# Optimization experiments

Hardware: AMD Instinct MI355X
Metric: run time of the kernel (lower is better)

Reference implementation:

```python
import jax, jax.numpy as jnp
import numpy as np

D_MODEL = 1024
N_HEADS = 16
HEAD_DIM = D_MODEL // N_HEADS


def setup_inputs() -> dict:
    key = jax.random.key(0)
    ks = jax.random.split(key, 9)
    B, S, D = 2, 2048, D_MODEL
    scale = 1.0 / np.sqrt(D)
    return {
        "q": jax.random.normal(ks[0], (B, S, D), jnp.float32),
        "k": jax.random.normal(ks[1], (B, S, D), jnp.float32),
        "v": jax.random.normal(ks[2], (B, S, D), jnp.float32),
        "Wq": jax.random.normal(ks[3], (D, D), jnp.float32) * scale,
        "bq": jax.random.normal(ks[4], (D,), jnp.float32) * 0.01,
        "Wk": jax.random.normal(ks[5], (D, D), jnp.float32) * scale,
        "bk": jax.random.normal(ks[6], (D,), jnp.float32) * 0.01,
        "Wv": jax.random.normal(ks[7], (D, D), jnp.float32) * scale,
        "bv": jax.random.normal(ks[8], (D,), jnp.float32) * 0.01,
    }


def reference(q, k, v, Wq, bq, Wk, bk, Wv, bv):
    B, S, D = q.shape
    H, Dh = N_HEADS, D // N_HEADS
    # linear projections (torch Linear: x @ W.T + b)
    qp = q @ Wq.T + bq
    kp = k @ Wk.T + bk
    vp = v @ Wv.T + bv
    # [B, S, H, Dh] -> [B, H, S, Dh]
    qh = qp.reshape(B, S, H, Dh).transpose(0, 2, 1, 3)
    kh = kp.reshape(B, S, H, Dh).transpose(0, 2, 1, 3)
    vh = vp.reshape(B, S, H, Dh).transpose(0, 2, 1, 3)
    # scaled dot-product attention (mask=None path)
    scores = jnp.einsum('bhqd,bhkd->bhqk', qh, kh) / jnp.sqrt(jnp.asarray(Dh, qh.dtype))
    attn = jax.nn.softmax(scores, axis=-1)
    out = jnp.einsum('bhqk,bhkd->bhqd', attn, vh)
    # [B, H, S, Dh] -> [B, S, D]
    return out.transpose(0, 2, 1, 3).reshape(B, S, D)
```

## Files before the change

### kernel.cpp

```cpp
#include <hip/hip_runtime.h>
#include <stdint.h>
#include <stddef.h>


#define NH  16
#define DH  64
#define SEQ 2048
#define DM  1024
#define NB  2

#define ACT_N (NB * SEQ * DM)
#define W_N   (DM * DM)
#define QSCALE 0.18033688011116012f

typedef float  f32x4  __attribute__((ext_vector_type(4)));
typedef __bf16 bf16x8 __attribute__((ext_vector_type(8)));
typedef __bf16 bf16x4 __attribute__((ext_vector_type(4)));

__device__ __forceinline__ __bf16 f2bf(float f) { return (__bf16)f; }

__device__ __forceinline__ float fexp2(float x) {
    float r; asm("v_exp_f32 %0, %1" : "=v"(r) : "v"(x)); return r;
}

__device__ __forceinline__ void gload_lds16(const void* g, void* l) {
    __builtin_amdgcn_global_load_lds(
        (const __attribute__((address_space(1))) void*)g,
        (__attribute__((address_space(3))) void*)l, 16, 0, 0);
}

__global__ __launch_bounds__(256) void cvt6(
    const float* __restrict__ s0, const float* __restrict__ s1,
    const float* __restrict__ s2, const float* __restrict__ s3,
    const float* __restrict__ s4, const float* __restrict__ s5,
    __bf16* __restrict__ d0, __bf16* __restrict__ d1, __bf16* __restrict__ d2,
    __bf16* __restrict__ d3, __bf16* __restrict__ d4, __bf16* __restrict__ d5)
{
    const float* s; __bf16* d; int n;
    switch (blockIdx.z) {
        case 0: s = s0; d = d0; n = ACT_N; break;
        case 1: s = s1; d = d1; n = ACT_N; break;
        case 2: s = s2; d = d2; n = ACT_N; break;
        case 3: s = s3; d = d3; n = W_N;   break;
        case 4: s = s4; d = d4; n = W_N;   break;
        default: s = s5; d = d5; n = W_N;  break;
    }
    const size_t i = ((size_t)blockIdx.x * 256 + threadIdx.x) * 8;
    if (i >= (size_t)n) return;
    float4 f0 = *(const float4*)(s + i);
    float4 f1 = *(const float4*)(s + i + 4);
    bf16x8 o;
    o[0] = f2bf(f0.x); o[1] = f2bf(f0.y); o[2] = f2bf(f0.z); o[3] = f2bf(f0.w);
    o[4] = f2bf(f1.x); o[5] = f2bf(f1.y); o[6] = f2bf(f1.z); o[7] = f2bf(f1.w);
    *(bf16x8*)(d + i) = o;
}

__global__ __launch_bounds__(256) void proj3(
    const __bf16* __restrict__ X0, const __bf16* __restrict__ X1, const __bf16* __restrict__ X2,
    const __bf16* __restrict__ W0, const __bf16* __restrict__ W1, const __bf16* __restrict__ W2,
    const float* __restrict__ b0, const float* __restrict__ b1, const float* __restrict__ b2,
    __bf16* __restrict__ dq, __bf16* __restrict__ dk, __bf16* __restrict__ dv)
{
    __shared__ __align__(16) __bf16 sA[128][32];
    __shared__ __align__(16) __bf16 sB[128][32];

    const __bf16 *X, *W; const float* bias; __bf16* dst;
    if (blockIdx.z == 0)      { X = X0; W = W0; bias = b0; dst = dq; }
    else if (blockIdx.z == 1) { X = X1; W = W1; bias = b1; dst = dk; }
    else                      { X = X2; W = W2; bias = b2; dst = dv; }
    const bool vpath = (blockIdx.z == 2);

    const int lane = threadIdx.x & 63;
    const int wv   = threadIdx.x >> 6;
    const int mb = blockIdx.x * 128;
    const int nb = blockIdx.y * 128;
    const int lm0 = (wv >> 1) * 64;
    const int ln0 = (wv & 1) * 64;
    const int lr = lane & 15;
    const int lg = lane >> 4;
    const int lk = lg * 8;
    const int srow = lane >> 2;
    const int scol = (lane & 3) * 8;

    f32x4 acc[4][4];
#pragma unroll
    for (int i = 0; i < 4; ++i)
#pragma unroll
        for (int j = 0; j < 4; ++j) acc[i][j] = (f32x4){0.f, 0.f, 0.f, 0.f};

    for (int k0 = 0; k0 < DM; k0 += 32) {
        __syncthreads();
#pragma unroll
        for (int c = wv * 2; c < wv * 2 + 2; ++c) {
            gload_lds16(X + (size_t)(mb + c * 16 + srow) * DM + k0 + scol, &sA[c * 16][0]);
            gload_lds16(W + (size_t)(nb + c * 16 + srow) * DM + k0 + scol, &sB[c * 16][0]);
        }
        __syncthreads();

        bf16x8 a[4], b[4];
#pragma unroll
        for (int t = 0; t < 4; ++t) {
            a[t] = *(const bf16x8*)&sA[lm0 + t * 16 + lr][lk];
            b[t] = *(const bf16x8*)&sB[ln0 + t * 16 + lr][lk];
        }
        if (!vpath) {
#pragma unroll
            for (int nt = 0; nt < 4; ++nt)
#pragma unroll
                for (int mt = 0; mt < 4; ++mt)
                    acc[nt][mt] = __builtin_amdgcn_mfma_f32_16x16x32_bf16(
                        b[nt], a[mt], acc[nt][mt], 0, 0, 0);
        } else {
#pragma unroll
            for (int mt = 0; mt < 4; ++mt)
#pragma unroll
                for (int nt = 0; nt < 4; ++nt)
                    acc[mt][nt] = __builtin_amdgcn_mfma_f32_16x16x32_bf16(
                        a[mt], b[nt], acc[mt][nt], 0, 0, 0);
        }
    }

    if (!vpath) {
        const float scale = (blockIdx.z == 0) ? QSCALE : 1.0f;
#pragma unroll
        for (int nt = 0; nt < 4; ++nt) {
            const int n_base = nb + ln0 + nt * 16 + lg * 4;
            const float4 bb = *(const float4*)&bias[n_base];
            const int h = n_base >> 6, dh = n_base & 63;
#pragma unroll
            for (int mt = 0; mt < 4; ++mt) {
                const int m_g = mb + lm0 + mt * 16 + lr;
                const int bi = m_g >> 11;
                const int s  = m_g & (SEQ - 1);
                bf16x4 w;
                w[0] = f2bf((acc[nt][mt][0] + bb.x) * scale);
                w[1] = f2bf((acc[nt][mt][1] + bb.y) * scale);
                w[2] = f2bf((acc[nt][mt][2] + bb.z) * scale);
                w[3] = f2bf((acc[nt][mt][3] + bb.w) * scale);
                *(bf16x4*)&dst[((size_t)((bi * NH + h) * SEQ + s)) * DH + dh] = w;
            }
        }
    } else {
        const int h = (nb + ln0) >> 6;
#pragma unroll
        for (int nt = 0; nt < 4; ++nt) {
            const int n_g = nb + ln0 + nt * 16 + lr;
            const float bb = bias[n_g];
            const int dh = n_g & 63;
#pragma unroll
            for (int mt = 0; mt < 4; ++mt) {
                const int m_g = mb + lm0 + mt * 16 + lg * 4;
                const int bi = m_g >> 11;
                const int s0 = m_g & (SEQ - 1);
                bf16x4 w;
#pragma unroll
                for (int r = 0; r < 4; ++r) w[r] = f2bf(acc[mt][nt][r] + bb);
                *(bf16x4*)&dst[((size_t)((bi * NH + h) * DH + dh)) * SEQ + s0] = w;
            }
        }
    }
}

__global__ __launch_bounds__(256) void attn_kernel(
    const __bf16* __restrict__ qh, const __bf16* __restrict__ kh,
    const __bf16* __restrict__ vT, float* __restrict__ out)
{
    __shared__ __align__(16) __bf16 kbuf[3][4096];
    __shared__ __align__(16) __bf16 vbuf[3][4096];

    const int tid  = threadIdx.x;
    const int lane = tid & 63;
    const int wv   = tid >> 6;
    const int i    = blockIdx.x;
    const int slot = i >> 3;
    const int bh   = (i & 7) * 4 + (slot >> 4);
    const int qt   = slot & 15;
    const size_t hb = (size_t)bh * SEQ * DH;
    const int q0 = qt * 128 + wv * 32;
    const int lq = lane & 15;
    const int lg = lane >> 4;
    const int swz = (lq & 7) << 4;

    const int p0 = tid, p1 = tid + 256;
    const int c0 = (p0 ^ ((p0 >> 3) & 7)) & 7;
    const int c1 = (p1 ^ ((p1 >> 3) & 7)) & 7;
    const int r0 = p0 >> 3, r1 = p1 >> 3;
    const int gr0 = (r0 & 35) | ((r0 & 12) << 1) | ((r0 & 16) >> 2);
    const int gr1 = (r1 & 35) | ((r1 & 12) << 1) | ((r1 & 16) >> 2);
    const __bf16* ks0 = kh + hb + (size_t)gr0 * DH + c0 * 8;
    const __bf16* ks1 = kh + hb + (size_t)gr1 * DH + c1 * 8;
    const __bf16* vs0 = vT + hb + (size_t)r0 * SEQ + c0 * 8;
    const __bf16* vs1 = vT + hb + (size_t)r1 * SEQ + c1 * 8;
    const int dst0 = wv * 512;
    const int dst1 = 2048 + wv * 512;

#define STAGE(SEL, TI) { \
    gload_lds16(ks0 + (size_t)(TI) * 64 * DH, &kbuf[SEL][dst0]); \
    gload_lds16(ks1 + (size_t)(TI) * 64 * DH, &kbuf[SEL][dst1]); \
    gload_lds16(vs0 + (TI) * 64, &vbuf[SEL][dst0]); \
    gload_lds16(vs1 + (TI) * 64, &vbuf[SEL][dst1]); }

    bf16x8 bQ[2][2];
#pragma unroll
    for (int qtf = 0; qtf < 2; ++qtf)
#pragma unroll
        for (int ks = 0; ks < 2; ++ks)
            bQ[qtf][ks] = *(const bf16x8*)(qh + hb +
                (size_t)(q0 + qtf * 16 + lq) * DH + ks * 32 + lg * 8);

    bf16x8 ONES;
#pragma unroll
    for (int e = 0; e < 8; ++e) ONES[e] = f2bf(1.0f);

    f32x4 O[2][4];
#pragma unroll
    for (int qtf = 0; qtf < 2; ++qtf)
#pragma unroll
        for (int dt = 0; dt < 4; ++dt) O[qtf][dt] = (f32x4){0.f, 0.f, 0.f, 0.f};
    f32x4 Ol[2];
    Ol[0] = (f32x4){0.f, 0.f, 0.f, 0.f};
    Ol[1] = (f32x4){0.f, 0.f, 0.f, 0.f};

    const int rdk0 = lq * 128 + ((0 * 64 + lg * 16) ^ swz);
    const int rdk1 = lq * 128 + ((1 * 64 + lg * 16) ^ swz);

    f32x4 scA[2][4], scB[2][4];
    bf16x8 paf[2][2];

#define QK(SL, SC) { \
    const char* kc = (const char*)&kbuf[SL][0]; \
    _Pragma("unroll") for (int kt = 0; kt < 4; ++kt) { \
        const bf16x8 ak0 = *(const bf16x8*)(kc + kt * 2048 + rdk0); \
        const bf16x8 ak1 = *(const bf16x8*)(kc + kt * 2048 + rdk1); \
        _Pragma("unroll") for (int qtf = 0; qtf < 2; ++qtf) { \
            f32x4 c = (f32x4){0.f, 0.f, 0.f, 0.f}; \
            c = __builtin_amdgcn_mfma_f32_16x16x32_bf16(ak0, bQ[qtf][0], c, 0, 0, 0); \
            c = __builtin_amdgcn_mfma_f32_16x16x32_bf16(ak1, bQ[qtf][1], c, 0, 0, 0); \
            SC[qtf][kt] = c; } } }

#define SMAX(SC) { \
    _Pragma("unroll") for (int qtf = 0; qtf < 2; ++qtf) \
    _Pragma("unroll") for (int ks = 0; ks < 2; ++ks) { \
        bf16x8 w; \
        _Pragma("unroll") for (int r = 0; r < 4; ++r) { \
            w[r]     = f2bf(fexp2(SC[qtf][2 * ks][r])); \
            w[4 + r] = f2bf(fexp2(SC[qtf][2 * ks + 1][r])); } \
        paf[qtf][ks] = w; } }

#define PV(SL) { \
    const char* vc = (const char*)&vbuf[SL][0]; \
    _Pragma("unroll") for (int ks = 0; ks < 2; ++ks) { \
        const int rd = (ks == 0) ? rdk0 : rdk1; \
        _Pragma("unroll") for (int dt = 0; dt < 4; ++dt) { \
            const bf16x8 bv = *(const bf16x8*)(vc + dt * 2048 + rd); \
            O[0][dt] = __builtin_amdgcn_mfma_f32_16x16x32_bf16(paf[0][ks], bv, O[0][dt], 0, 0, 0); \
            O[1][dt] = __builtin_amdgcn_mfma_f32_16x16x32_bf16(paf[1][ks], bv, O[1][dt], 0, 0, 0); } \
        Ol[0] = __builtin_amdgcn_mfma_f32_16x16x32_bf16(paf[0][ks], ONES, Ol[0], 0, 0, 0); \
        Ol[1] = __builtin_amdgcn_mfma_f32_16x16x32_bf16(paf[1][ks], ONES, Ol[1], 0, 0, 0); } }

#define BODY(T, SCUR, SNXT) { \
    SMAX(SCUR); \
    __syncthreads(); \
    if ((T) + 2 < 32) STAGE(((T) + 2) % 3, (T) + 2); \
    __builtin_amdgcn_s_setprio(1); \
    if ((T) + 1 < 32) QK(((T) + 1) % 3, SNXT); \
    PV((T) % 3); \
    __builtin_amdgcn_s_setprio(0); }

    STAGE(0, 0);
    STAGE(1, 1);
    __syncthreads();
    QK(0, scA);

#pragma unroll
    for (int t = 0; t < 32; t += 2) {
        BODY(t, scA, scB);
        BODY(t + 1, scB, scA);
    }
#undef BODY
#undef PV
#undef SMAX
#undef QK
#undef STAGE

    const int b = bh >> 4, h = bh & 15;
#pragma unroll
    for (int qtf = 0; qtf < 2; ++qtf) {
#pragma unroll
        for (int r = 0; r < 4; ++r) {
            const float li = 1.0f / (qtf ? Ol[1][r] : Ol[0][r]);
            const int s_g = q0 + qtf * 16 + lg * 4 + r;
            float* op = out + ((size_t)(b * SEQ + s_g)) * DM + h * DH;
#pragma unroll
            for (int dt = 0; dt < 4; ++dt)
                op[dt * 16 + lq] = O[qtf][dt][r] * li;
        }
    }
}

extern "C" void kernel_launch(void* const* d_in, const int* in_sizes, int n_in,
                              void* d_out, int out_size, void* d_ws, size_t ws_size,
                              hipStream_t stream)
{
    (void)in_sizes; (void)n_in; (void)out_size; (void)ws_size;
    const float* q  = (const float*)d_in[0];
    const float* k  = (const float*)d_in[1];
    const float* v  = (const float*)d_in[2];
    const float* Wq = (const float*)d_in[3];
    const float* bq = (const float*)d_in[4];
    const float* Wk = (const float*)d_in[5];
    const float* bk = (const float*)d_in[6];
    const float* Wv = (const float*)d_in[7];
    const float* bv = (const float*)d_in[8];

    const size_t act = (size_t)ACT_N;
    const size_t wn  = (size_t)W_N;
    __bf16* qx  = (__bf16*)d_ws;
    __bf16* kx  = qx + act;
    __bf16* vx  = kx + act;
    __bf16* wqb = vx + act;
    __bf16* wkb = wqb + wn;
    __bf16* wvb = wkb + wn;
    __bf16* qhd = wvb + wn;
    __bf16* khd = qhd + act;
    __bf16* vhd = khd + act;
    float* out = (float*)d_out;

    cvt6<<<dim3(2048, 1, 6), dim3(256), 0, stream>>>(
        q, k, v, Wq, Wk, Wv, qx, kx, vx, wqb, wkb, wvb);
    proj3<<<dim3(32, 8, 3), dim3(256), 0, stream>>>(
        qx, kx, vx, wqb, wkb, wvb, bq, bk, bv, qhd, khd, vhd);
    attn_kernel<<<dim3(512), dim3(256), 0, stream>>>(qhd, khd, vhd, out);
}
```

Before: 102.6 us.

## Rewrite projection GEMM with 256x256 tiles, double-buffered LDS and swizzle

The QKV projection kernel moves from 128x128 tiles with K=32 steps to 256x256 tiles with K=64 steps across 8 waves. It double-buffers LDS, XOR-swizzles the LDS layout to avoid bank conflicts, and interleaves async global-to-LDS loads for the next tile with MFMA on the current one, using setprio around the MFMA groups. The aim is more data reuse per load, fewer barriers, and hiding load latency in the projection stage. In exchange it uses much more LDS and registers, so occupancy drops, and the grid shrinks to 192 blocks, which may underfill the GPU's CUs.

```diff
diff --git a/kernel.cpp b/kernel.cpp
--- a/kernel.cpp
+++ b/kernel.cpp
@@ -55,106 +55,158 @@
     *(bf16x8*)(d + i) = o;
 }
 
-__global__ __launch_bounds__(256) void proj3(
-    const __bf16* __restrict__ X0, const __bf16* __restrict__ X1, const __bf16* __restrict__ X2,
-    const __bf16* __restrict__ W0, const __bf16* __restrict__ W1, const __bf16* __restrict__ W2,
-    const float* __restrict__ b0, const float* __restrict__ b1, const float* __restrict__ b2,
+__global__ __launch_bounds__(512) void proj3(
+    const __bf16* __restrict__ Xq, const __bf16* __restrict__ Xk, const __bf16* __restrict__ Xv,
+    const __bf16* __restrict__ Wq, const __bf16* __restrict__ Wk, const __bf16* __restrict__ Wv,
+    const float* __restrict__ bq, const float* __restrict__ bk, const float* __restrict__ bv,
     __bf16* __restrict__ dq, __bf16* __restrict__ dk, __bf16* __restrict__ dv)
 {
-    __shared__ __align__(16) __bf16 sA[128][32];
-    __shared__ __align__(16) __bf16 sB[128][32];
+    __shared__ __align__(16) __bf16 sA[2][16384];
+    __shared__ __align__(16) __bf16 sB[2][16384];
+
+    const int tid  = threadIdx.x;
+    const int lane = tid & 63;
+    const int wv   = tid >> 6;
+    const int wm   = wv >> 2;
+    const int wn   = wv & 3;
+    const int tensor = blockIdx.y >> 2;
+    const int nb   = (blockIdx.y & 3) * 256;
+    const int mb   = blockIdx.x * 256;
 
     const __bf16 *X, *W; const float* bias; __bf16* dst;
-    if (blockIdx.z == 0)      { X = X0; W = W0; bias = b0; dst = dq; }
-    else if (blockIdx.z == 1) { X = X1; W = W1; bias = b1; dst = dk; }
-    else                      { X = X2; W = W2; bias = b2; dst = dv; }
-    const bool vpath = (blockIdx.z == 2);
-
-    const int lane = threadIdx.x & 63;
-    const int wv   = threadIdx.x >> 6;
-    const int mb = blockIdx.x * 128;
-    const int nb = blockIdx.y * 128;
-    const int lm0 = (wv >> 1) * 64;
-    const int ln0 = (wv & 1) * 64;
+    if (tensor == 0)      { X = Xq; W = Wq; bias = bq; dst = dq; }
+    else if (tensor == 1) { X = Xk; W = Wk; bias = bk; dst = dk; }
+    else                  { X = Xv; W = Wv; bias = bv; dst = dv; }
+    const bool vpath = (tensor == 2);
+
     const int lr = lane & 15;
     const int lg = lane >> 4;
-    const int lk = lg * 8;
-    const int srow = lane >> 2;
-    const int scol = (lane & 3) * 8;
-
-    f32x4 acc[4][4];
-#pragma unroll
-    for (int i = 0; i < 4; ++i)
-#pragma unroll
-        for (int j = 0; j < 4; ++j) acc[i][j] = (f32x4){0.f, 0.f, 0.f, 0.f};
-
-    for (int k0 = 0; k0 < DM; k0 += 32) {
-        __syncthreads();
-#pragma unroll
-        for (int c = wv * 2; c < wv * 2 + 2; ++c) {
-            gload_lds16(X + (size_t)(mb + c * 16 + srow) * DM + k0 + scol, &sA[c * 16][0]);
-            gload_lds16(W + (size_t)(nb + c * 16 + srow) * DM + k0 + scol, &sB[c * 16][0]);
+
+    const int srow = lane >> 3;
+    const int gch  = (lane & 7) ^ srow;
+    const __bf16* xs = X + (size_t)(mb + wv * 32 + srow) * DM + gch * 8;
+    const __bf16* ws = W + (size_t)(nb + wv * 32 + srow) * DM + gch * 8;
+
+#define LA(BUF, T, I) gload_lds16(xs + (size_t)(T) * 64 + (size_t)(I) * 8 * DM, \
+                                  &sA[BUF][(wv * 32 + (I) * 8) * 64])
+#define LB(BUF, T, I) gload_lds16(ws + (size_t)(T) * 64 + (size_t)(I) * 8 * DM, \
+                                  &sB[BUF][(wv * 32 + (I) * 8) * 64])
+
+    const int rsw = (lr & 7) << 4;
+    const int rdk0 = (0 * 64 + lg * 16) ^ rsw;
+    const int rdk1 = (1 * 64 + lg * 16) ^ rsw;
+    const int arow = (wm * 128 + lr) * 128;
+    const int brow = (wn * 64 + lr) * 128;
+
+    f32x4 acc[32];
+#pragma unroll
+    for (int i = 0; i < 32; ++i) acc[i] = (f32x4){0.f, 0.f, 0.f, 0.f};
+
+    bf16x8 aP[4], aQ2[4], bP[4], bQ2[4];
+
+#define RDA(R, CA, MH, KS) { \
+    _Pragma("unroll") for (int mt = 0; mt < 4; ++mt) \
+        R[mt] = *(const bf16x8*)((CA) + arow + ((MH) * 4 + mt) * 16 * 128 + ((KS) ? rdk1 : rdk0)); }
+#define RDB(R, CB, KS) { \
+    _Pragma("unroll") for (int nt = 0; nt < 4; ++nt) \
+        R[nt] = *(const bf16x8*)((CB) + brow + nt * 16 * 128 + ((KS) ? rdk1 : rdk0)); }
+
+#define MFMAQ(MH, AA, BB) { \
+    __builtin_amdgcn_s_setprio(1); \
+    if (!vpath) { \
+        _Pragma("unroll") for (int nt = 0; nt < 4; ++nt) \
+        _Pragma("unroll") for (int mt = 0; mt < 4; ++mt) \
+            acc[nt * 8 + (MH) * 4 + mt] = __builtin_amdgcn_mfma_f32_16x16x32_bf16( \
+                BB[nt], AA[mt], acc[nt * 8 + (MH) * 4 + mt], 0, 0, 0); \
+    } else { \
+        _Pragma("unroll") for (int mt = 0; mt < 4; ++mt) \
+        _Pragma("unroll") for (int nt = 0; nt < 4; ++nt) \
+            acc[((MH) * 4 + mt) * 4 + nt] = __builtin_amdgcn_mfma_f32_16x16x32_bf16( \
+                AA[mt], BB[nt], acc[((MH) * 4 + mt) * 4 + nt], 0, 0, 0); } \
+    __builtin_amdgcn_s_setprio(0); }
+
+#pragma unroll
+    for (int i = 0; i < 4; ++i) { LA(0, 0, i); LB(0, 0, i); }
+    __syncthreads();
+    {
+        const char* ca = (const char*)&sA[0][0];
+        const char* cb = (const char*)&sB[0][0];
+        RDA(aP, ca, 0, 0);
+        RDB(bP, cb, 0);
+    }
+
+#pragma unroll
+    for (int t = 0; t < 16; ++t) {
+        const int cur = t & 1, nxt = cur ^ 1;
+        const char* ca = (const char*)&sA[cur][0];
+        const char* cb = (const char*)&sB[cur][0];
+        const char* caN = (const char*)&sA[nxt][0];
+        const char* cbN = (const char*)&sB[nxt][0];
+        const bool more = (t + 1 < 16);
+
+        if (more) { LA(nxt, t + 1, 0); LA(nxt, t + 1, 1); LB(nxt, t + 1, 0); }
+        RDA(aQ2, ca, 1, 0);
+        MFMAQ(0, aP, bP);
+
+        if (more) { LA(nxt, t + 1, 2); LA(nxt, t + 1, 3); LB(nxt, t + 1, 1); }
+        RDA(aP, ca, 0, 1);
+        RDB(bQ2, cb, 1);
+        MFMAQ(1, aQ2, bP);
+
+        if (more) { LB(nxt, t + 1, 2); LB(nxt, t + 1, 3); }
+        RDA(aQ2, ca, 1, 1);
+        MFMAQ(0, aP, bQ2);
+
+        MFMAQ(1, aQ2, bQ2);
+        if (more) {
+            __syncthreads();
+            RDA(aP, caN, 0, 0);
+            RDB(bP, cbN, 0);
         }
-        __syncthreads();
-
-        bf16x8 a[4], b[4];
-#pragma unroll
-        for (int t = 0; t < 4; ++t) {
-            a[t] = *(const bf16x8*)&sA[lm0 + t * 16 + lr][lk];
-            b[t] = *(const bf16x8*)&sB[ln0 + t * 16 + lr][lk];
-        }
-        if (!vpath) {
-#pragma unroll
-            for (int nt = 0; nt < 4; ++nt)
-#pragma unroll
-                for (int mt = 0; mt < 4; ++mt)
-                    acc[nt][mt] = __builtin_amdgcn_mfma_f32_16x16x32_bf16(
-                        b[nt], a[mt], acc[nt][mt], 0, 0, 0);
-        } else {
-#pragma unroll
-            for (int mt = 0; mt < 4; ++mt)
-#pragma unroll
-                for (int nt = 0; nt < 4; ++nt)
-                    acc[mt][nt] = __builtin_amdgcn_mfma_f32_16x16x32_bf16(
-                        a[mt], b[nt], acc[mt][nt], 0, 0, 0);
-        }
-    }
+    }
+#undef MFMAQ
+#undef RDA
+#undef RDB
+#undef LA
+#undef LB
 
     if (!vpath) {
-        const float scale = (blockIdx.z == 0) ? QSCALE : 1.0f;
+        const float scale = (tensor == 0) ? QSCALE : 1.0f;
 #pragma unroll
         for (int nt = 0; nt < 4; ++nt) {
-            const int n_base = nb + ln0 + nt * 16 + lg * 4;
+            const int n_base = nb + wn * 64 + nt * 16 + lg * 4;
             const float4 bb = *(const float4*)&bias[n_base];
             const int h = n_base >> 6, dh = n_base & 63;
 #pragma unroll
-            for (int mt = 0; mt < 4; ++mt) {
-                const int m_g = mb + lm0 + mt * 16 + lr;
+            for (int mt = 0; mt < 8; ++mt) {
+                const int m_g = mb + wm * 128 + mt * 16 + lr;
                 const int bi = m_g >> 11;
                 const int s  = m_g & (SEQ - 1);
+                const f32x4 v = acc[nt * 8 + mt];
                 bf16x4 w;
-                w[0] = f2bf((acc[nt][mt][0] + bb.x) * scale);
-                w[1] = f2bf((acc[nt][mt][1] + bb.y) * scale);
-                w[2] = f2bf((acc[nt][mt][2] + bb.z) * scale);
-                w[3] = f2bf((acc[nt][mt][3] + bb.w) * scale);
+                w[0] = f2bf((v[0] + bb.x) * scale);
+                w[1] = f2bf((v[1] + bb.y) * scale);
+                w[2] = f2bf((v[2] + bb.z) * scale);
+                w[3] = f2bf((v[3] + bb.w) * scale);
                 *(bf16x4*)&dst[((size_t)((bi * NH + h) * SEQ + s)) * DH + dh] = w;
             }
         }
     } else {
-        const int h = (nb + ln0) >> 6;
+        const int h = (nb + wn * 64) >> 6;
 #pragma unroll
         for (int nt = 0; nt < 4; ++nt) {
-            const int n_g = nb + ln0 + nt * 16 + lr;
+            const int n_g = nb + wn * 64 + nt * 16 + lr;
             const float bb = bias[n_g];
             const int dh = n_g & 63;
 #pragma unroll
-            for (int mt = 0; mt < 4; ++mt) {
-                const int m_g = mb + lm0 + mt * 16 + lg * 4;
+            for (int mt = 0; mt < 8; ++mt) {
+                const int m_g = mb + wm * 128 + mt * 16 + lg * 4;
                 const int bi = m_g >> 11;
                 const int s0 = m_g & (SEQ - 1);
+                const f32x4 v = acc[mt * 4 + nt];
                 bf16x4 w;
 #pragma unroll
-                for (int r = 0; r < 4; ++r) w[r] = f2bf(acc[mt][nt][r] + bb);
+                for (int r = 0; r < 4; ++r) w[r] = f2bf(v[r] + bb);
                 *(bf16x4*)&dst[((size_t)((bi * NH + h) * DH + dh)) * SEQ + s0] = w;
             }
         }
@@ -328,7 +380,7 @@
 
     cvt6<<<dim3(2048, 1, 6), dim3(256), 0, stream>>>(
         q, k, v, Wq, Wk, Wv, qx, kx, vx, wqb, wkb, wvb);
-    proj3<<<dim3(32, 8, 3), dim3(256), 0, stream>>>(
+    proj3<<<dim3(16, 12), dim3(512), 0, stream>>>(
         qx, kx, vx, wqb, wkb, wvb, bq, bk, bv, qhd, khd, vhd);
     attn_kernel<<<dim3(512), dim3(256), 0, stream>>>(qhd, khd, vhd, out);
 }
```

New measurement: 90.09 us, median of 2. 1.14x faster.
